# Performance work log

Measured on AMD Instinct MI355X. Metric: run time of the kernel, lower is better.

Reference implementation:

```python
import jax, jax.numpy as jnp
import numpy as np

B, D, H = 65536, 128, 64


def setup_inputs() -> dict:
    key = jax.random.key(0)
    ks = jax.random.split(key, 20)
    p = lambda k, shp, fan: jax.random.normal(k, shp, jnp.float32) * (1.0 / np.sqrt(fan))
    return {
        "l": jax.random.normal(ks[0], (B, D), jnp.float32),
        "a": jax.random.normal(ks[1], (B, D), jnp.float32),
        "v": jax.random.normal(ks[2], (B, D), jnp.float32),
        "att_w": p(ks[3], (D, 1), D), "att_b": jnp.zeros((1,), jnp.float32),
        "gf_w1": p(ks[4], (2 * D, H), 2 * D), "gf_b1": jnp.zeros((H,), jnp.float32),
        "gf_w2": p(ks[5], (H, D), H), "gf_b2": jnp.zeros((D,), jnp.float32),
        "gf2_w1": p(ks[6], (2 * D, H), 2 * D), "gf2_b1": jnp.zeros((H,), jnp.float32),
        "gf2_w2": p(ks[7], (H, D), H), "gf2_b2": jnp.zeros((D,), jnp.float32),
        "ll_w1": p(ks[8], (3 * D, H), 3 * D), "ll_b1": jnp.zeros((H,), jnp.float32),
        "ll_w2": p(ks[9], (H, H), H), "ll_b2": jnp.zeros((H,), jnp.float32),
        "ll_w3": p(ks[10], (H, D), H), "ll_b3": jnp.zeros((D,), jnp.float32),
    }


def reference(l, a, v, att_w, att_b, gf_w1, gf_b1, gf_w2, gf_b2,
              gf2_w1, gf2_b1, gf2_w2, gf2_b2,
              ll_w1, ll_b1, ll_w2, ll_b2, ll_w3, ll_b3):
    def gf(x, y):  # graph_fusion on cat([x,y],1): Linear->LeakyReLU(0.2)->Linear->Tanh
        h = jnp.concatenate([x, y], 1) @ gf_w1 + gf_b1
        h = jax.nn.leaky_relu(h, 0.2)
        return jnp.tanh(h @ gf_w2 + gf_b2)

    def gf2(x, y):
        h = jnp.concatenate([x, y], 1) @ gf2_w1 + gf2_b1
        h = jax.nn.leaky_relu(h, 0.2)
        return jnp.tanh(h @ gf2_w2 + gf2_b2)

    dot = lambda x, y: jnp.sum(x * y, axis=1)  # batched [B,1,d]@[B,d,1] -> [B]

    sa = jnp.tanh(a @ att_w + att_b)  # [B,1]
    sv = jnp.tanh(v @ att_w + att_b)
    sl = jnp.tanh(l @ att_w + att_b)

    unimodal = (sa * a + sv * v + sl * l) / 3.0  # [B,D]
    sa1, sv1, sl1 = sa[:, 0], sv[:, 0], sl[:, 0]

    # modalities are overwritten by softmax in the original
    a = jax.nn.softmax(a, axis=1)
    v = jax.nn.softmax(v, axis=1)
    l = jax.nn.softmax(l, axis=1)

    sav = (sa1 + sv1) / (dot(a, v) + 0.5)
    sal = (sa1 + sl1) / (dot(a, l) + 0.5)
    svl = (sl1 + sv1) / (dot(v, l) + 0.5)
    normalize = jax.nn.softmax(jnp.stack([sav, sal, svl], axis=1), axis=1)  # [B,3]

    gav, gal, gvl = gf(a, v), gf(a, l), gf(v, l)  # reused (torch computes twice)
    a_v = jnp.tanh(normalize[:, 0:1] * gav)
    a_l = jnp.tanh(normalize[:, 1:2] * gal)
    v_l = jnp.tanh(normalize[:, 2:3] * gvl)
    bimodal = a_v + a_l + v_l

    a_v2 = jax.nn.softmax(gav, axis=1)
    a_l2 = jax.nn.softmax(gal, axis=1)
    v_l2 = jax.nn.softmax(gvl, axis=1)

    savvl = (sav + svl) / (dot(a_v2, v_l2) + 0.5)
    saavl = (sav + sal) / (dot(a_v2, a_l2) + 0.5)
    savll = (sal + svl) / (dot(a_l2, v_l2) + 0.5)
    savl = (sav + sl1) / (dot(a_v2, l) + 0.5)
    salv = (sal + sv1) / (dot(a_l2, v) + 0.5)
    svla = (sa1 + svl) / (dot(v_l2, a) + 0.5)
    n2 = jax.nn.softmax(jnp.stack([savvl, saavl, savll, savl, salv, svla], axis=1), axis=1)

    trimodal = (jnp.tanh(n2[:, 0:1] * gf2(a_v, v_l))
                + jnp.tanh(n2[:, 1:2] * gf2(a_v, a_l))
                + jnp.tanh(n2[:, 2:3] * gf2(v_l, a_l))
                + jnp.tanh(n2[:, 3:4] * gf2(a_v, l))
                + jnp.tanh(n2[:, 4:5] * gf2(a_l, v))
                + jnp.tanh(n2[:, 5:6] * gf2(v_l, a)))

    fusion = jnp.concatenate([unimodal, bimodal, trimodal], axis=1)  # [B,3D]
    h = jnp.tanh(fusion @ ll_w1 + ll_b1)
    h = jnp.tanh(h @ ll_w2 + ll_b2)
    return jnp.tanh(h @ ll_w3 + ll_b3)
```

## Files before the change

### kernel.cpp

```cpp
#include <hip/hip_runtime.h>

typedef short bfrag __attribute__((ext_vector_type(8)));
typedef float facc  __attribute__((ext_vector_type(4)));
typedef unsigned short u16;
typedef unsigned int   u32;

#define LOG2E 1.4426950408889634f
#define K2E   2.8853900817779268f
#define MFMA(A,B,C) __builtin_amdgcn_mfma_f32_16x16x32_bf16((A),(B),(C),0,0,0)

__device__ __forceinline__ void bar_lds(){
  asm volatile("s_waitcnt lgkmcnt(0)" ::: "memory");
  __builtin_amdgcn_s_barrier();
}

#define AS_E 0
#define VS_E 2176
#define LS_E 4352
#define AV_E 6528
#define AL_E 8704
#define VL_E 10880
#define HH_E 13056
#define SCR_B 39936
#define SM_BYTES 40704

__device__ __forceinline__ float ex2(float x){ return __builtin_amdgcn_exp2f(x); }
__device__ __forceinline__ float rcpf_(float x){ return __builtin_amdgcn_rcpf(x); }
__device__ __forceinline__ float ftanh_s(float y){ return 1.0f - 2.0f*rcpf_(ex2(y) + 1.0f); }
__device__ __forceinline__ float ftanhb(float y){
  float y2 = y*y, y4 = y2*y2;
  float n = (y2*105.f + 945.f) + y4;
  float d = (y2*420.f + 945.f) + y4*15.f;
  return y*n*rcpf_(d);
}
__device__ __forceinline__ u16 f2b(float x){ return (u16)((__float_as_uint(x) + 0x8000u)>>16); }
__device__ __forceinline__ float b2f(u16 b){ return __uint_as_float(((u32)b)<<16); }
__device__ __forceinline__ u32 pk2(float x0, float x1){
  return __builtin_amdgcn_perm(__float_as_uint(x1)+0x8000u, __float_as_uint(x0)+0x8000u, 0x07060302u);
}
template<int N>
__device__ __forceinline__ float ror16f(float v){
  return __int_as_float(__builtin_amdgcn_update_dpp(0, __float_as_int(v), 0x120|N, 0xF, 0xF, false));
}
__device__ __forceinline__ float rsum16(float v){
  v += ror16f<8>(v); v += ror16f<4>(v); v += ror16f<2>(v); v += ror16f<1>(v); return v;
}
__device__ __forceinline__ void st4b(u16* p, float x0,float x1,float x2,float x3){
  *(uint2*)p = make_uint2(pk2(x0,x1), pk2(x2,x3));
}

__global__ void prep_weights(const float* __restrict__ gf_w1, const float* __restrict__ gf_w2,
                             const float* __restrict__ gf2_w1, const float* __restrict__ gf2_w2,
                             const float* __restrict__ ll_w1, const float* __restrict__ ll_w2,
                             const float* __restrict__ ll_w3, u16* __restrict__ blob)
{
  u32 i = blockIdx.x*256u + threadIdx.x;
  if (i >= 86016u) return;
  u32 off, K, ln; const float* src;
  if      (i < 16384u){ off=0u;     K=256u; ln=6u; src=gf_w1; }
  else if (i < 24576u){ off=16384u; K=64u;  ln=7u; src=gf_w2; }
  else if (i < 40960u){ off=24576u; K=256u; ln=6u; src=gf2_w1; }
  else if (i < 49152u){ off=40960u; K=64u;  ln=7u; src=gf2_w2; }
  else if (i < 73728u){ off=49152u; K=384u; ln=6u; src=ll_w1; }
  else if (i < 77824u){ off=73728u; K=64u;  ln=6u; src=ll_w2; }
  else               { off=77824u; K=64u;  ln=7u; src=ll_w3; }
  u32 li = i - off;
  u32 k = li >> ln, n = li & ((1u<<ln)-1u);
  blob[off + n*K + k] = f2b(src[li]);
}

__global__ __launch_bounds__(256,4) void fused_graph(
    const float* __restrict__ Lg, const float* __restrict__ Ag, const float* __restrict__ Vg,
    const float* __restrict__ att_w, const float* __restrict__ att_b,
    const float* __restrict__ gf_b1, const float* __restrict__ gf_b2,
    const float* __restrict__ gf2_b1, const float* __restrict__ gf2_b2,
    const float* __restrict__ ll_b1, const float* __restrict__ ll_b2, const float* __restrict__ ll_b3,
    const u16* __restrict__ wb, float* __restrict__ out)
{
  __shared__ alignas(16) char sm[SM_BYTES];
  u16* smu = (u16*)sm;
  float* scr = (float*)(sm + SCR_B);

  const int tid = threadIdx.x;
  const int lane = tid & 63;
  const int w = tid >> 6;
  const int m = lane & 15;
  const int q = lane >> 4;
  const int er = tid >> 4;
  const int ep = tid & 15;
  const int row0 = blockIdx.x << 4;

  const int gb = (row0 + er)*128 + ep*4;
  facc A0 = *(const facc*)(Ag+gb), A1 = *(const facc*)(Ag+gb+64);
  facc V0 = *(const facc*)(Vg+gb), V1 = *(const facc*)(Vg+gb+64);
  facc L0 = *(const facc*)(Lg+gb), L1 = *(const facc*)(Lg+gb+64);
  facc W0 = *(const facc*)(att_w+ep*4), W1 = *(const facc*)(att_w+ep*4+64);
  float abK = att_b[0]*K2E;
  float pa=0.f,pv=0.f,pl=0.f;
  #pragma unroll
  for (int i=0;i<4;i++){ pa += A0[i]*W0[i]+A1[i]*W1[i]; pv += V0[i]*W0[i]+V1[i]*W1[i]; pl += L0[i]*W0[i]+L1[i]*W1[i]; }
  float sa = ftanh_s(rsum16(pa)*K2E + abK);
  float sv = ftanh_s(rsum16(pv)*K2E + abK);
  float sl = ftanh_s(rsum16(pl)*K2E + abK);
  u32 uni_pk[4];
  {
    const float th = 1.0f/3.0f;
    uni_pk[0] = pk2((sa*A0[0]+sv*V0[0]+sl*L0[0])*th, (sa*A0[1]+sv*V0[1]+sl*L0[1])*th);
    uni_pk[1] = pk2((sa*A0[2]+sv*V0[2]+sl*L0[2])*th, (sa*A0[3]+sv*V0[3]+sl*L0[3])*th);
    uni_pk[2] = pk2((sa*A1[0]+sv*V1[0]+sl*L1[0])*th, (sa*A1[1]+sv*V1[1]+sl*L1[1])*th);
    uni_pk[3] = pk2((sa*A1[2]+sv*V1[2]+sl*L1[2])*th, (sa*A1[3]+sv*V1[3]+sl*L1[3])*th);
  }
  #define SMAX(X0,X1,OFFE) { \
    float s_=0.f; \
    _Pragma("unroll") for (int i=0;i<4;i++){ X0[i]=ex2(X0[i]*LOG2E); X1[i]=ex2(X1[i]*LOG2E); s_+=X0[i]+X1[i]; } \
    s_ = rsum16(s_); float rs_ = rcpf_(s_); \
    _Pragma("unroll") for (int i=0;i<4;i++){ X0[i]*=rs_; X1[i]*=rs_; } \
    u16* dp_ = smu + (OFFE) + er*136 + ep*4; \
    st4b(dp_, X0[0],X0[1],X0[2],X0[3]); st4b(dp_+64, X1[0],X1[1],X1[2],X1[3]); }
  SMAX(A0,A1,AS_E)
  SMAX(V0,V1,VS_E)
  SMAX(L0,L1,LS_E)
  float dav=0.f,dal=0.f,dvl=0.f;
  #pragma unroll
  for (int i=0;i<4;i++){ dav += A0[i]*V0[i]+A1[i]*V1[i]; dal += A0[i]*L0[i]+A1[i]*L1[i]; dvl += V0[i]*L0[i]+V1[i]*L1[i]; }
  dav = rsum16(dav); dal = rsum16(dal); dvl = rsum16(dvl);
  float sav = (sa+sv)*rcpf_(dav+0.5f);
  float sal = (sa+sl)*rcpf_(dal+0.5f);
  float svl = (sl+sv)*rcpf_(dvl+0.5f);
  if (ep==0){
    float e0 = ex2(sav*LOG2E), e1 = ex2(sal*LOG2E), e2 = ex2(svl*LOG2E);
    float rs = rcpf_(e0+e1+e2);
    scr[er*12+0]=e0*rs; scr[er*12+1]=e1*rs; scr[er*12+2]=e2*rs;
  }
  bar_lds();

  const u16* g1t = wb;
  const u16* g2t = wb + 16384;
  bfrag B1[8];
  #pragma unroll
  for (int s=0;s<8;s++) B1[s] = *(const bfrag*)(g1t + (w*16+m)*256 + s*32 + q*8);
  facc acc0={0,0,0,0}, acc1={0,0,0,0}, acc2={0,0,0,0};
  #pragma unroll
  for (int s=0;s<8;s++){
    int k = s*32 + q*8, ko = k & 127; bool hi = (k >= 128);
    const u16* p0 = smu + (hi? VS_E:AS_E) + m*136 + ko;
    const u16* p1 = smu + (hi? LS_E:AS_E) + m*136 + ko;
    const u16* p2 = smu + (hi? LS_E:VS_E) + m*136 + ko;
    acc0 = MFMA(*(const bfrag*)p0, B1[s], acc0);
    acc1 = MFMA(*(const bfrag*)p1, B1[s], acc1);
    acc2 = MFMA(*(const bfrag*)p2, B1[s], acc2);
  }
  {
    float b1v = gf_b1[w*16+m];
    #pragma unroll
    for (int r=0;r<4;r++){
      int rr = q*4+r;
      float h0 = acc0[r]+b1v; h0 = fmaxf(h0, 0.2f*h0);
      float h1 = acc1[r]+b1v; h1 = fmaxf(h1, 0.2f*h1);
      float h2 = acc2[r]+b1v; h2 = fmaxf(h2, 0.2f*h2);
      smu[HH_E + 0*1152 + rr*72 + w*16+m] = f2b(h0);
      smu[HH_E + 1*1152 + rr*72 + w*16+m] = f2b(h1);
      smu[HH_E + 2*1152 + rr*72 + w*16+m] = f2b(h2);
    }
  }
  bar_lds();
  facc c2[3][2] = {{{0,0,0,0},{0,0,0,0}},{{0,0,0,0},{0,0,0,0}},{{0,0,0,0},{0,0,0,0}}};
  #pragma unroll
  for (int s=0;s<2;s++){
    int k = s*32 + q*8;
    bfrag Af0 = *(const bfrag*)(smu + HH_E + 0*1152 + m*72 + k);
    bfrag Af1 = *(const bfrag*)(smu + HH_E + 1*1152 + m*72 + k);
    bfrag Af2 = *(const bfrag*)(smu + HH_E + 2*1152 + m*72 + k);
    #pragma unroll
    for (int t=0;t<2;t++){
      bfrag B2f = *(const bfrag*)(g2t + ((w+4*t)*16+m)*64 + s*32 + q*8);
      c2[0][t] = MFMA(Af0, B2f, c2[0][t]);
      c2[1][t] = MFMA(Af1, B2f, c2[1][t]);
      c2[2][t] = MFMA(Af2, B2f, c2[2][t]);
    }
  }
  {
    float b2v0s = gf_b2[w*16+m]*K2E, b2v1s = gf_b2[(w+4)*16+m]*K2E;
    #pragma unroll
    for (int p3=0;p3<3;p3++){
      #pragma unroll
      for (int t=0;t<2;t++){
        float bbs = t? b2v1s : b2v0s;
        int cc = (w+4*t)*16+m;
        #pragma unroll
        for (int r=0;r<4;r++){
          smu[AV_E + p3*2176 + (q*4+r)*136 + cc] = f2b(ftanh_s(c2[p3][t][r]*K2E + bbs));
        }
      }
    }
  }
  bar_lds();

  float E0[8], E1[8], E2[8], bim8[8];
  float RS0, RS1, RS2;
  #pragma unroll
  for (int j=0;j<8;j++) bim8[j]=0.f;
  #define GSTATC(EA, G3, RS) { \
    u16* gpa_ = smu + AV_E + (G3)*2176 + er*136 + ep*4; \
    u16* gpb_ = gpa_ + 64; \
    ushort4 ga_ = *(const ushort4*)gpa_; ushort4 gb_ = *(const ushort4*)gpb_; \
    float x_[8]; \
    x_[0]=b2f(ga_.x); x_[1]=b2f(ga_.y); x_[2]=b2f(ga_.z); x_[3]=b2f(ga_.w); \
    x_[4]=b2f(gb_.x); x_[5]=b2f(gb_.y); x_[6]=b2f(gb_.z); x_[7]=b2f(gb_.w); \
    float nn_ = scr[er*12+(G3)]; \
    float t_[8]; \
    _Pragma("unroll") for (int j=0;j<8;j++){ t_[j]=ftanhb(nn_*x_[j]); bim8[j]+=t_[j]; } \
    st4b(gpa_, t_[0],t_[1],t_[2],t_[3]); \
    st4b(gpb_, t_[4],t_[5],t_[6],t_[7]); \
    float s_=0.f; \
    _Pragma("unroll") for (int j=0;j<8;j++){ x_[j]=ex2(x_[j]*LOG2E); s_+=x_[j]; } \
    s_ = rsum16(s_); RS = rcpf_(s_); \
    _Pragma("unroll") for (int j=0;j<8;j++) EA[j]=x_[j]; }
  GSTATC(E0,0,RS0)
  GSTATC(E1,1,RS1)
  GSTATC(E2,2,RS2)
  float d01=0.f,d02=0.f,d12=0.f,d0l=0.f,d1v=0.f,d2a=0.f;
  #pragma unroll
  for (int i=0;i<4;i++){
    d01 += E0[i]*E1[i] + E0[4+i]*E1[4+i];
    d02 += E0[i]*E2[i] + E0[4+i]*E2[4+i];
    d12 += E1[i]*E2[i] + E1[4+i]*E2[4+i];
    d0l += E0[i]*L0[i] + E0[4+i]*L1[i];
    d1v += E1[i]*V0[i] + E1[4+i]*V1[i];
    d2a += E2[i]*A0[i] + E2[4+i]*A1[i];
  }
  d01=rsum16(d01)*(RS0*RS1); d02=rsum16(d02)*(RS0*RS2); d12=rsum16(d12)*(RS1*RS2);
  d0l=rsum16(d0l)*RS0;       d1v=rsum16(d1v)*RS1;       d2a=rsum16(d2a)*RS2;
  if (ep==0){
    float x0 = (sav+svl)*rcpf_(d02+0.5f);
    float x1 = (sav+sal)*rcpf_(d01+0.5f);
    float x2 = (sal+svl)*rcpf_(d12+0.5f);
    float x3 = (sav+sl )*rcpf_(d0l+0.5f);
    float x4 = (sal+sv )*rcpf_(d1v+0.5f);
    float x5 = (sa +svl)*rcpf_(d2a+0.5f);
    float e0=ex2(x0*LOG2E), e1=ex2(x1*LOG2E), e2=ex2(x2*LOG2E);
    float e3=ex2(x3*LOG2E), e4=ex2(x4*LOG2E), e5=ex2(x5*LOG2E);
    float rs = rcpf_(e0+e1+e2+e3+e4+e5);
    scr[er*12+4]=e0*rs; scr[er*12+5]=e1*rs; scr[er*12+6]=e2*rs;
    scr[er*12+7]=e3*rs; scr[er*12+8]=e4*rs; scr[er*12+9]=e5*rs;
  }
  bar_lds();

  const u16* h1t = wb + 24576;
  const u16* h2t = wb + 40960;
  bfrag C1[8];
  #pragma unroll
  for (int s=0;s<8;s++) C1[s] = *(const bfrag*)(h1t + (w*16+m)*256 + s*32 + q*8);
  const int S0[6] = {AV_E, AV_E, VL_E, AV_E, AL_E, VL_E};
  const int S1[6] = {VL_E, AL_E, AL_E, LS_E, VS_E, AS_E};
  facc cc1[6];
  #pragma unroll
  for (int pr=0;pr<6;pr++){ facc z = {0,0,0,0}; cc1[pr] = z; }
  #pragma unroll
  for (int s=0;s<8;s++){
    int k = s*32+q*8, ko = k&127; bool hi = (k>=128);
    #pragma unroll
    for (int pr=0;pr<6;pr++){
      const u16* sp = smu + (hi? S1[pr]:S0[pr]) + m*136 + ko;
      cc1[pr] = MFMA(*(const bfrag*)sp, C1[s], cc1[pr]);
    }
  }
  {
    float b1v = gf2_b1[w*16+m];
    #pragma unroll
    for (int pr=0;pr<6;pr++){
      #pragma unroll
      for (int r=0;r<4;r++){
        float h = cc1[pr][r]+b1v; h = fmaxf(h,0.2f*h);
        smu[HH_E + pr*1152 + (q*4+r)*72 + w*16+m] = f2b(h);
      }
    }
  }
  bar_lds();
  facc cc2[6][2];
  #pragma unroll
  for (int pr=0;pr<6;pr++){ facc z = {0,0,0,0}; cc2[pr][0]=z; cc2[pr][1]=z; }
  #pragma unroll
  for (int s=0;s<2;s++){
    int k=s*32+q*8;
    bfrag Af[6];
    #pragma unroll
    for (int pr=0;pr<6;pr++) Af[pr] = *(const bfrag*)(smu + HH_E + pr*1152 + m*72 + k);
    #pragma unroll
    for (int t=0;t<2;t++){
      bfrag C2f = *(const bfrag*)(h2t + ((w+4*t)*16+m)*64 + s*32 + q*8);
      #pragma unroll
      for (int pr=0;pr<6;pr++) cc2[pr][t] = MFMA(Af[pr], C2f, cc2[pr][t]);
    }
  }
  {
    float b2v0s = gf2_b2[w*16+m]*K2E, b2v1s = gf2_b2[(w+4)*16+m]*K2E;
    float tri[2][4] = {{0,0,0,0},{0,0,0,0}};
    float n2v[4][6];
    #pragma unroll
    for (int r=0;r<4;r++){
      const float4 v4 = *(const float4*)(scr + (q*4+r)*12 + 4);
      const float2 v2 = *(const float2*)(scr + (q*4+r)*12 + 8);
      n2v[r][0]=v4.x; n2v[r][1]=v4.y; n2v[r][2]=v4.z; n2v[r][3]=v4.w;
      n2v[r][4]=v2.x; n2v[r][5]=v2.y;
    }
    #pragma unroll
    for (int pr=0;pr<6;pr++){
      #pragma unroll
      for (int t=0;t<2;t++){
        float bbs = t? b2v1s : b2v0s;
        #pragma unroll
        for (int r=0;r<4;r++){
          float g = ftanh_s(cc2[pr][t][r]*K2E + bbs);
          tri[t][r] += ftanhb(n2v[r][pr]*g);
        }
      }
    }
    #pragma unroll
    for (int t=0;t<2;t++){
      #pragma unroll
      for (int r=0;r<4;r++){
        smu[LS_E + (q*4+r)*136 + (w+4*t)*16+m] = f2b(tri[t][r]);
      }
    }
    u16* vp = smu + VS_E + er*136 + ep*4;
    st4b(vp,    bim8[0],bim8[1],bim8[2],bim8[3]);
    st4b(vp+64, bim8[4],bim8[5],bim8[6],bim8[7]);
    *(uint2*)(smu + AS_E + er*136 + ep*4)      = make_uint2(uni_pk[0], uni_pk[1]);
    *(uint2*)(smu + AS_E + er*136 + ep*4 + 64) = make_uint2(uni_pk[2], uni_pk[3]);
  }
  bar_lds();

  const u16* lw1 = wb + 49152;
  const u16* lw2 = wb + 73728;
  const u16* lw3 = wb + 77824;
  {
    facc c = {0,0,0,0};
    #pragma unroll
    for (int s=0;s<12;s++){
      const int base = (s<4)? AS_E : (s<8)? VS_E : LS_E;
      bfrag Bf = *(const bfrag*)(lw1 + (w*16+m)*384 + s*32 + q*8);
      bfrag Af = *(const bfrag*)(smu + base + m*136 + (s&3)*32 + q*8);
      c = MFMA(Af, Bf, c);
    }
    float bs = ll_b1[w*16+m]*K2E;
    #pragma unroll
    for (int r=0;r<4;r++) smu[HH_E + (q*4+r)*72 + w*16+m] = f2b(ftanh_s(c[r]*K2E + bs));
  }
  bar_lds();
  {
    facc c = {0,0,0,0};
    #pragma unroll
    for (int s=0;s<2;s++){
      bfrag Bf = *(const bfrag*)(lw2 + (w*16+m)*64 + s*32 + q*8);
      bfrag Af = *(const bfrag*)(smu + HH_E + m*72 + s*32 + q*8);
      c = MFMA(Af, Bf, c);
    }
    float bs = ll_b2[w*16+m]*K2E;
    #pragma unroll
    for (int r=0;r<4;r++) smu[HH_E + 1152 + (q*4+r)*72 + w*16+m] = f2b(ftanh_s(c[r]*K2E + bs));
  }
  bar_lds();
  {
    facc c0={0,0,0,0}, c1={0,0,0,0};
    #pragma unroll
    for (int s=0;s<2;s++){
      bfrag Af  = *(const bfrag*)(smu + HH_E + 1152 + m*72 + s*32 + q*8);
      bfrag Bf0 = *(const bfrag*)(lw3 + (w*16+m)*64 + s*32 + q*8);
      bfrag Bf1 = *(const bfrag*)(lw3 + ((w+4)*16+m)*64 + s*32 + q*8);
      c0 = MFMA(Af, Bf0, c0);
      c1 = MFMA(Af, Bf1, c1);
    }
    float b0s = ll_b3[w*16+m]*K2E, b1s = ll_b3[(w+4)*16+m]*K2E;
    #pragma unroll
    for (int r=0;r<4;r++){
      out[(row0+q*4+r)*128 + w*16+m]        = ftanh_s(c0[r]*K2E + b0s);
      out[(row0+q*4+r)*128 + (w+4)*16+m]    = ftanh_s(c1[r]*K2E + b1s);
    }
  }
}

extern "C" void kernel_launch(void* const* d_in, const int* in_sizes, int n_in,
                              void* d_out, int out_size, void* d_ws, size_t ws_size,
                              hipStream_t stream)
{
  const float* l      = (const float*)d_in[0];
  const float* a      = (const float*)d_in[1];
  const float* v      = (const float*)d_in[2];
  const float* att_w  = (const float*)d_in[3];
  const float* att_b  = (const float*)d_in[4];
  const float* gf_w1  = (const float*)d_in[5];
  const float* gf_b1  = (const float*)d_in[6];
  const float* gf_w2  = (const float*)d_in[7];
  const float* gf_b2  = (const float*)d_in[8];
  const float* gf2_w1 = (const float*)d_in[9];
  const float* gf2_b1 = (const float*)d_in[10];
  const float* gf2_w2 = (const float*)d_in[11];
  const float* gf2_b2 = (const float*)d_in[12];
  const float* ll_w1  = (const float*)d_in[13];
  const float* ll_b1  = (const float*)d_in[14];
  const float* ll_w2  = (const float*)d_in[15];
  const float* ll_b2  = (const float*)d_in[16];
  const float* ll_w3  = (const float*)d_in[17];
  const float* ll_b3  = (const float*)d_in[18];
  u16* blob = (u16*)d_ws;

  prep_weights<<<336, 256, 0, stream>>>(gf_w1, gf_w2, gf2_w1, gf2_w2, ll_w1, ll_w2, ll_w3, blob);
  fused_graph<<<4096, 256, 0, stream>>>(l, a, v, att_w, att_b,
                                        gf_b1, gf_b2, gf2_b1, gf2_b2,
                                        ll_b1, ll_b2, ll_b3, blob, (float*)d_out);
}
```

Baseline: 246.4 us.

## Process 32 rows per 512-thread block with XOR-swizzled LDS layouts

Doubles the rows per block to 32, using 8 waves split into two row tiles by four column groups, and halves the grid. Padded LDS strides are replaced with XOR swizzles to avoid bank conflicts. The six trimodal GEMM pairs now run in two passes of three, which cuts the hidden-buffer LDS footprint and adds one extra barrier. LDS per block grows to about 62 KB, which may lower the number of resident blocks per CU.

```diff
diff --git a/kernel.cpp b/kernel.cpp
--- a/kernel.cpp
+++ b/kernel.cpp
@@ -15,14 +15,14 @@
 }
 
 #define AS_E 0
-#define VS_E 2176
-#define LS_E 4352
-#define AV_E 6528
-#define AL_E 8704
-#define VL_E 10880
-#define HH_E 13056
-#define SCR_B 39936
-#define SM_BYTES 40704
+#define VS_E 4096
+#define LS_E 8192
+#define AV_E 12288
+#define AL_E 16384
+#define VL_E 20480
+#define H3_E 24576
+#define SCR_B 61440
+#define SM_BYTES 62976
 
 __device__ __forceinline__ float ex2(float x){ return __builtin_amdgcn_exp2f(x); }
 __device__ __forceinline__ float rcpf_(float x){ return __builtin_amdgcn_rcpf(x); }
@@ -38,6 +38,9 @@
 __device__ __forceinline__ u32 pk2(float x0, float x1){
   return __builtin_amdgcn_perm(__float_as_uint(x1)+0x8000u, __float_as_uint(x0)+0x8000u, 0x07060302u);
 }
+__device__ __forceinline__ int fsw(int row, int col){ return (row*128 + col) ^ ((row&15)<<3); }
+__device__ __forceinline__ int hsw(int row, int col){ return (row*64 + col) ^ ((row&7)<<3) ^ ((row&8)<<1); }
+
 template<int N>
 __device__ __forceinline__ float ror16f(float v){
   return __int_as_float(__builtin_amdgcn_update_dpp(0, __float_as_int(v), 0x120|N, 0xF, 0xF, false));
@@ -69,7 +72,7 @@
   blob[off + n*K + k] = f2b(src[li]);
 }
 
-__global__ __launch_bounds__(256,4) void fused_graph(
+__global__ __launch_bounds__(512,4) void fused_graph(
     const float* __restrict__ Lg, const float* __restrict__ Ag, const float* __restrict__ Vg,
     const float* __restrict__ att_w, const float* __restrict__ att_b,
     const float* __restrict__ gf_b1, const float* __restrict__ gf_b2,
@@ -84,11 +87,13 @@
   const int tid = threadIdx.x;
   const int lane = tid & 63;
   const int w = tid >> 6;
+  const int rt = w >> 2;
+  const int cw = w & 3;
   const int m = lane & 15;
   const int q = lane >> 4;
   const int er = tid >> 4;
   const int ep = tid & 15;
-  const int row0 = blockIdx.x << 4;
+  const int row0 = blockIdx.x << 5;
 
   const int gb = (row0 + er)*128 + ep*4;
   facc A0 = *(const facc*)(Ag+gb), A1 = *(const facc*)(Ag+gb+64);
@@ -115,8 +120,8 @@
     _Pragma("unroll") for (int i=0;i<4;i++){ X0[i]=ex2(X0[i]*LOG2E); X1[i]=ex2(X1[i]*LOG2E); s_+=X0[i]+X1[i]; } \
     s_ = rsum16(s_); float rs_ = rcpf_(s_); \
     _Pragma("unroll") for (int i=0;i<4;i++){ X0[i]*=rs_; X1[i]*=rs_; } \
-    u16* dp_ = smu + (OFFE) + er*136 + ep*4; \
-    st4b(dp_, X0[0],X0[1],X0[2],X0[3]); st4b(dp_+64, X1[0],X1[1],X1[2],X1[3]); }
+    st4b(smu + (OFFE) + fsw(er, ep*4),    X0[0],X0[1],X0[2],X0[3]); \
+    st4b(smu + (OFFE) + fsw(er, ep*4+64), X1[0],X1[1],X1[2],X1[3]); }
   SMAX(A0,A1,AS_E)
   SMAX(V0,V1,VS_E)
   SMAX(L0,L1,LS_E)
@@ -138,29 +143,29 @@
   const u16* g2t = wb + 16384;
   bfrag B1[8];
   #pragma unroll
-  for (int s=0;s<8;s++) B1[s] = *(const bfrag*)(g1t + (w*16+m)*256 + s*32 + q*8);
+  for (int s=0;s<8;s++) B1[s] = *(const bfrag*)(g1t + (cw*16+m)*256 + s*32 + q*8);
   facc acc0={0,0,0,0}, acc1={0,0,0,0}, acc2={0,0,0,0};
   #pragma unroll
   for (int s=0;s<8;s++){
     int k = s*32 + q*8, ko = k & 127; bool hi = (k >= 128);
-    const u16* p0 = smu + (hi? VS_E:AS_E) + m*136 + ko;
-    const u16* p1 = smu + (hi? LS_E:AS_E) + m*136 + ko;
-    const u16* p2 = smu + (hi? LS_E:VS_E) + m*136 + ko;
+    const u16* p0 = smu + (hi? VS_E:AS_E) + fsw(rt*16+m, ko);
+    const u16* p1 = smu + (hi? LS_E:AS_E) + fsw(rt*16+m, ko);
+    const u16* p2 = smu + (hi? LS_E:VS_E) + fsw(rt*16+m, ko);
     acc0 = MFMA(*(const bfrag*)p0, B1[s], acc0);
     acc1 = MFMA(*(const bfrag*)p1, B1[s], acc1);
     acc2 = MFMA(*(const bfrag*)p2, B1[s], acc2);
   }
   {
-    float b1v = gf_b1[w*16+m];
+    float b1v = gf_b1[cw*16+m];
     #pragma unroll
     for (int r=0;r<4;r++){
-      int rr = q*4+r;
+      int rr = rt*16 + q*4+r;
       float h0 = acc0[r]+b1v; h0 = fmaxf(h0, 0.2f*h0);
       float h1 = acc1[r]+b1v; h1 = fmaxf(h1, 0.2f*h1);
       float h2 = acc2[r]+b1v; h2 = fmaxf(h2, 0.2f*h2);
-      smu[HH_E + 0*1152 + rr*72 + w*16+m] = f2b(h0);
-      smu[HH_E + 1*1152 + rr*72 + w*16+m] = f2b(h1);
-      smu[HH_E + 2*1152 + rr*72 + w*16+m] = f2b(h2);
+      smu[H3_E + 0*2048 + hsw(rr, cw*16+m)] = f2b(h0);
+      smu[H3_E + 1*2048 + hsw(rr, cw*16+m)] = f2b(h1);
+      smu[H3_E + 2*2048 + hsw(rr, cw*16+m)] = f2b(h2);
     }
   }
   bar_lds();
@@ -168,28 +173,28 @@
   #pragma unroll
   for (int s=0;s<2;s++){
     int k = s*32 + q*8;
-    bfrag Af0 = *(const bfrag*)(smu + HH_E + 0*1152 + m*72 + k);
-    bfrag Af1 = *(const bfrag*)(smu + HH_E + 1*1152 + m*72 + k);
-    bfrag Af2 = *(const bfrag*)(smu + HH_E + 2*1152 + m*72 + k);
+    bfrag Af0 = *(const bfrag*)(smu + H3_E + 0*2048 + hsw(rt*16+m, k));
+    bfrag Af1 = *(const bfrag*)(smu + H3_E + 1*2048 + hsw(rt*16+m, k));
+    bfrag Af2 = *(const bfrag*)(smu + H3_E + 2*2048 + hsw(rt*16+m, k));
     #pragma unroll
     for (int t=0;t<2;t++){
-      bfrag B2f = *(const bfrag*)(g2t + ((w+4*t)*16+m)*64 + s*32 + q*8);
+      bfrag B2f = *(const bfrag*)(g2t + ((cw+4*t)*16+m)*64 + s*32 + q*8);
       c2[0][t] = MFMA(Af0, B2f, c2[0][t]);
       c2[1][t] = MFMA(Af1, B2f, c2[1][t]);
       c2[2][t] = MFMA(Af2, B2f, c2[2][t]);
     }
   }
   {
-    float b2v0s = gf_b2[w*16+m]*K2E, b2v1s = gf_b2[(w+4)*16+m]*K2E;
+    float b2v0s = gf_b2[cw*16+m]*K2E, b2v1s = gf_b2[(cw+4)*16+m]*K2E;
     #pragma unroll
     for (int p3=0;p3<3;p3++){
       #pragma unroll
       for (int t=0;t<2;t++){
         float bbs = t? b2v1s : b2v0s;
-        int cc = (w+4*t)*16+m;
+        int cc = (cw+4*t)*16+m;
         #pragma unroll
         for (int r=0;r<4;r++){
-          smu[AV_E + p3*2176 + (q*4+r)*136 + cc] = f2b(ftanh_s(c2[p3][t][r]*K2E + bbs));
+          smu[AV_E + p3*4096 + fsw(rt*16 + q*4+r, cc)] = f2b(ftanh_s(c2[p3][t][r]*K2E + bbs));
         }
       }
     }
@@ -201,8 +206,8 @@
   #pragma unroll
   for (int j=0;j<8;j++) bim8[j]=0.f;
   #define GSTATC(EA, G3, RS) { \
-    u16* gpa_ = smu + AV_E + (G3)*2176 + er*136 + ep*4; \
-    u16* gpb_ = gpa_ + 64; \
+    u16* gpa_ = smu + AV_E + (G3)*4096 + fsw(er, ep*4); \
+    u16* gpb_ = smu + AV_E + (G3)*4096 + fsw(er, ep*4+64); \
     ushort4 ga_ = *(const ushort4*)gpa_; ushort4 gb_ = *(const ushort4*)gpb_; \
     float x_[8]; \
     x_[0]=b2f(ga_.x); x_[1]=b2f(ga_.y); x_[2]=b2f(ga_.z); x_[3]=b2f(ga_.w); \
@@ -250,84 +255,80 @@
   const u16* h2t = wb + 40960;
   bfrag C1[8];
   #pragma unroll
-  for (int s=0;s<8;s++) C1[s] = *(const bfrag*)(h1t + (w*16+m)*256 + s*32 + q*8);
-  const int S0[6] = {AV_E, AV_E, VL_E, AV_E, AL_E, VL_E};
-  const int S1[6] = {VL_E, AL_E, AL_E, LS_E, VS_E, AS_E};
-  facc cc1[6];
-  #pragma unroll
-  for (int pr=0;pr<6;pr++){ facc z = {0,0,0,0}; cc1[pr] = z; }
-  #pragma unroll
-  for (int s=0;s<8;s++){
-    int k = s*32+q*8, ko = k&127; bool hi = (k>=128);
-    #pragma unroll
-    for (int pr=0;pr<6;pr++){
-      const u16* sp = smu + (hi? S1[pr]:S0[pr]) + m*136 + ko;
-      cc1[pr] = MFMA(*(const bfrag*)sp, C1[s], cc1[pr]);
-    }
-  }
-  {
-    float b1v = gf2_b1[w*16+m];
-    #pragma unroll
-    for (int pr=0;pr<6;pr++){
+  for (int s=0;s<8;s++) C1[s] = *(const bfrag*)(h1t + (cw*16+m)*256 + s*32 + q*8);
+  const int PB0[6] = {AV_E, AV_E, VL_E, AV_E, AL_E, VL_E};
+  const int PB1[6] = {VL_E, AL_E, AL_E, LS_E, VS_E, AS_E};
+  float tri[2][4] = {{0,0,0,0},{0,0,0,0}};
+  float b1v2 = gf2_b1[cw*16+m];
+  float b2v0s = gf2_b2[cw*16+m]*K2E, b2v1s = gf2_b2[(cw+4)*16+m]*K2E;
+  #pragma unroll
+  for (int ps=0; ps<2; ps++){
+    facc cc1[3];
+    #pragma unroll
+    for (int pl=0;pl<3;pl++){ facc z = {0,0,0,0}; cc1[pl] = z; }
+    #pragma unroll
+    for (int s=0;s<8;s++){
+      int k = s*32+q*8, ko = k&127; bool hi = (k>=128);
+      #pragma unroll
+      for (int pl=0;pl<3;pl++){
+        int pr = ps*3+pl;
+        const u16* sp = smu + (hi? PB1[pr]:PB0[pr]) + fsw(rt*16+m, ko);
+        cc1[pl] = MFMA(*(const bfrag*)sp, C1[s], cc1[pl]);
+      }
+    }
+    #pragma unroll
+    for (int pl=0;pl<3;pl++){
       #pragma unroll
       for (int r=0;r<4;r++){
-        float h = cc1[pr][r]+b1v; h = fmaxf(h,0.2f*h);
-        smu[HH_E + pr*1152 + (q*4+r)*72 + w*16+m] = f2b(h);
-      }
-    }
-  }
-  bar_lds();
-  facc cc2[6][2];
-  #pragma unroll
-  for (int pr=0;pr<6;pr++){ facc z = {0,0,0,0}; cc2[pr][0]=z; cc2[pr][1]=z; }
-  #pragma unroll
-  for (int s=0;s<2;s++){
-    int k=s*32+q*8;
-    bfrag Af[6];
-    #pragma unroll
-    for (int pr=0;pr<6;pr++) Af[pr] = *(const bfrag*)(smu + HH_E + pr*1152 + m*72 + k);
-    #pragma unroll
-    for (int t=0;t<2;t++){
-      bfrag C2f = *(const bfrag*)(h2t + ((w+4*t)*16+m)*64 + s*32 + q*8);
-      #pragma unroll
-      for (int pr=0;pr<6;pr++) cc2[pr][t] = MFMA(Af[pr], C2f, cc2[pr][t]);
-    }
-  }
-  {
-    float b2v0s = gf2_b2[w*16+m]*K2E, b2v1s = gf2_b2[(w+4)*16+m]*K2E;
-    float tri[2][4] = {{0,0,0,0},{0,0,0,0}};
-    float n2v[4][6];
-    #pragma unroll
-    for (int r=0;r<4;r++){
-      const float4 v4 = *(const float4*)(scr + (q*4+r)*12 + 4);
-      const float2 v2 = *(const float2*)(scr + (q*4+r)*12 + 8);
-      n2v[r][0]=v4.x; n2v[r][1]=v4.y; n2v[r][2]=v4.z; n2v[r][3]=v4.w;
-      n2v[r][4]=v2.x; n2v[r][5]=v2.y;
-    }
-    #pragma unroll
-    for (int pr=0;pr<6;pr++){
+        float h = cc1[pl][r]+b1v2; h = fmaxf(h,0.2f*h);
+        smu[H3_E + pl*2048 + hsw(rt*16 + q*4+r, cw*16+m)] = f2b(h);
+      }
+    }
+    bar_lds();
+    facc cc2[3][2];
+    #pragma unroll
+    for (int pl=0;pl<3;pl++){ facc z = {0,0,0,0}; cc2[pl][0]=z; cc2[pl][1]=z; }
+    #pragma unroll
+    for (int s=0;s<2;s++){
+      int k=s*32+q*8;
+      bfrag Af0 = *(const bfrag*)(smu + H3_E + 0*2048 + hsw(rt*16+m, k));
+      bfrag Af1 = *(const bfrag*)(smu + H3_E + 1*2048 + hsw(rt*16+m, k));
+      bfrag Af2 = *(const bfrag*)(smu + H3_E + 2*2048 + hsw(rt*16+m, k));
+      #pragma unroll
+      for (int t=0;t<2;t++){
+        bfrag C2f = *(const bfrag*)(h2t + ((cw+4*t)*16+m)*64 + s*32 + q*8);
+        cc2[0][t] = MFMA(Af0, C2f, cc2[0][t]);
+        cc2[1][t] = MFMA(Af1, C2f, cc2[1][t]);
+        cc2[2][t] = MFMA(Af2, C2f, cc2[2][t]);
+      }
+    }
+    #pragma unroll
+    for (int pl=0;pl<3;pl++){
       #pragma unroll
       for (int t=0;t<2;t++){
         float bbs = t? b2v1s : b2v0s;
         #pragma unroll
         for (int r=0;r<4;r++){
-          float g = ftanh_s(cc2[pr][t][r]*K2E + bbs);
-          tri[t][r] += ftanhb(n2v[r][pr]*g);
+          float g = ftanh_s(cc2[pl][t][r]*K2E + bbs);
+          float nn = scr[(rt*16 + q*4+r)*12 + 4 + ps*3+pl];
+          tri[t][r] += ftanhb(nn*g);
         }
       }
     }
+    if (ps==0) bar_lds();
+  }
+  {
     #pragma unroll
     for (int t=0;t<2;t++){
       #pragma unroll
       for (int r=0;r<4;r++){
-        smu[LS_E + (q*4+r)*136 + (w+4*t)*16+m] = f2b(tri[t][r]);
-      }
-    }
-    u16* vp = smu + VS_E + er*136 + ep*4;
-    st4b(vp,    bim8[0],bim8[1],bim8[2],bim8[3]);
-    st4b(vp+64, bim8[4],bim8[5],bim8[6],bim8[7]);
-    *(uint2*)(smu + AS_E + er*136 + ep*4)      = make_uint2(uni_pk[0], uni_pk[1]);
-    *(uint2*)(smu + AS_E + er*136 + ep*4 + 64) = make_uint2(uni_pk[2], uni_pk[3]);
+        smu[LS_E + fsw(rt*16 + q*4+r, (cw+4*t)*16+m)] = f2b(tri[t][r]);
+      }
+    }
+    st4b(smu + VS_E + fsw(er, ep*4),    bim8[0],bim8[1],bim8[2],bim8[3]);
+    st4b(smu + VS_E + fsw(er, ep*4+64), bim8[4],bim8[5],bim8[6],bim8[7]);
+    *(uint2*)(smu + AS_E + fsw(er, ep*4))    = make_uint2(uni_pk[0], uni_pk[1]);
+    *(uint2*)(smu + AS_E + fsw(er, ep*4+64)) = make_uint2(uni_pk[2], uni_pk[3]);
   }
   bar_lds();
 
@@ -339,43 +340,45 @@
     #pragma unroll
     for (int s=0;s<12;s++){
       const int base = (s<4)? AS_E : (s<8)? VS_E : LS_E;
-      bfrag Bf = *(const bfrag*)(lw1 + (w*16+m)*384 + s*32 + q*8);
-      bfrag Af = *(const bfrag*)(smu + base + m*136 + (s&3)*32 + q*8);
+      bfrag Bf = *(const bfrag*)(lw1 + (cw*16+m)*384 + s*32 + q*8);
+      bfrag Af = *(const bfrag*)(smu + base + fsw(rt*16+m, (s&3)*32 + q*8));
       c = MFMA(Af, Bf, c);
     }
-    float bs = ll_b1[w*16+m]*K2E;
-    #pragma unroll
-    for (int r=0;r<4;r++) smu[HH_E + (q*4+r)*72 + w*16+m] = f2b(ftanh_s(c[r]*K2E + bs));
+    float bs = ll_b1[cw*16+m]*K2E;
+    #pragma unroll
+    for (int r=0;r<4;r++)
+      smu[H3_E + hsw(rt*16 + q*4+r, cw*16+m)] = f2b(ftanh_s(c[r]*K2E + bs));
   }
   bar_lds();
   {
     facc c = {0,0,0,0};
     #pragma unroll
     for (int s=0;s<2;s++){
-      bfrag Bf = *(const bfrag*)(lw2 + (w*16+m)*64 + s*32 + q*8);
-      bfrag Af = *(const bfrag*)(smu + HH_E + m*72 + s*32 + q*8);
+      bfrag Bf = *(const bfrag*)(lw2 + (cw*16+m)*64 + s*32 + q*8);
+      bfrag Af = *(const bfrag*)(smu + H3_E + hsw(rt*16+m, s*32 + q*8));
       c = MFMA(Af, Bf, c);
     }
-    float bs = ll_b2[w*16+m]*K2E;
-    #pragma unroll
-    for (int r=0;r<4;r++) smu[HH_E + 1152 + (q*4+r)*72 + w*16+m] = f2b(ftanh_s(c[r]*K2E + bs));
+    float bs = ll_b2[cw*16+m]*K2E;
+    #pragma unroll
+    for (int r=0;r<4;r++)
+      smu[H3_E + 2048 + hsw(rt*16 + q*4+r, cw*16+m)] = f2b(ftanh_s(c[r]*K2E + bs));
   }
   bar_lds();
   {
     facc c0={0,0,0,0}, c1={0,0,0,0};
     #pragma unroll
     for (int s=0;s<2;s++){
-      bfrag Af  = *(const bfrag*)(smu + HH_E + 1152 + m*72 + s*32 + q*8);
-      bfrag Bf0 = *(const bfrag*)(lw3 + (w*16+m)*64 + s*32 + q*8);
-      bfrag Bf1 = *(const bfrag*)(lw3 + ((w+4)*16+m)*64 + s*32 + q*8);
+      bfrag Af  = *(const bfrag*)(smu + H3_E + 2048 + hsw(rt*16+m, s*32 + q*8));
+      bfrag Bf0 = *(const bfrag*)(lw3 + (cw*16+m)*64 + s*32 + q*8);
+      bfrag Bf1 = *(const bfrag*)(lw3 + ((cw+4)*16+m)*64 + s*32 + q*8);
       c0 = MFMA(Af, Bf0, c0);
       c1 = MFMA(Af, Bf1, c1);
     }
-    float b0s = ll_b3[w*16+m]*K2E, b1s = ll_b3[(w+4)*16+m]*K2E;
+    float b0s = ll_b3[cw*16+m]*K2E, b1s = ll_b3[(cw+4)*16+m]*K2E;
     #pragma unroll
     for (int r=0;r<4;r++){
-      out[(row0+q*4+r)*128 + w*16+m]        = ftanh_s(c0[r]*K2E + b0s);
-      out[(row0+q*4+r)*128 + (w+4)*16+m]    = ftanh_s(c1[r]*K2E + b1s);
+      out[(row0 + rt*16 + q*4+r)*128 + cw*16+m]     = ftanh_s(c0[r]*K2E + b0s);
+      out[(row0 + rt*16 + q*4+r)*128 + (cw+4)*16+m] = ftanh_s(c1[r]*K2E + b1s);
     }
   }
 }
@@ -406,7 +409,7 @@
   u16* blob = (u16*)d_ws;
 
   prep_weights<<<336, 256, 0, stream>>>(gf_w1, gf_w2, gf2_w1, gf2_w2, ll_w1, ll_w2, ll_w3, blob);
-  fused_graph<<<4096, 256, 0, stream>>>(l, a, v, att_w, att_b,
+  fused_graph<<<2048, 512, 0, stream>>>(l, a, v, att_w, att_b,
                                         gf_b1, gf_b2, gf2_b1, gf2_b2,
                                         ll_b1, ll_b2, ll_b3, blob, (float*)d_out);
 }
```

New measurement: 314.8 us. 27.8% more time.
